# Kernel tuning notes

Measured on AMD Instinct MI355X. Metric: run time of the kernel, lower is better.

The kernel has to match this reference:

```python
import jax, jax.numpy as jnp
import numpy as np

B, H, W, K = 256, 28, 28, 5

def grid_edges_np(nb, h, w):
    # directed 8-neighbor edges on an h x w grid, replicated for nb graphs
    idx = np.arange(h * w).reshape(h, w)
    src_l, dst_l = [], []
    for dy in (-1, 0, 1):
        for dx in (-1, 0, 1):
            if dy == 0 and dx == 0:
                continue
            s = idx[max(0, -dy):h - max(0, dy), max(0, -dx):w - max(0, dx)]
            d = idx[max(0, dy):h - max(0, -dy), max(0, dx):w - max(0, -dx)]
            src_l.append(s.ravel()); dst_l.append(d.ravel())
    e = np.stack([np.concatenate(src_l), np.concatenate(dst_l)])
    off = np.arange(nb) * h * w
    return (e[:, None, :] + off[None, :, None]).reshape(2, -1).astype(np.int32)

def cart_pseudo(pos, src, dst):
    # CartesianAdj: relative offsets normalized into [0,1]^2
    cart = pos[dst] - pos[src]
    return cart / (2.0 * jnp.max(jnp.abs(cart))) + 0.5

def spline_conv(x, src, dst, pseudo, Wk, root, bias):
    # SplineConv, dim=2, kernel_size=K, degree-1 open B-splines, mean aggregation
    n = x.shape[0]
    v = jnp.clip(pseudo, 0.0, 1.0) * (K - 1)
    i0 = jnp.clip(jnp.floor(v), 0, K - 1).astype(jnp.int32)
    frac = v - i0.astype(v.dtype)
    i1 = jnp.minimum(i0 + 1, K - 1)
    Y = jnp.einsum('nf,kfg->nkg', x, Wk)  # [N, K*K, Fout]
    msg = 0.0
    for ia, ba in ((i0[:, 0], 1.0 - frac[:, 0]), (i1[:, 0], frac[:, 0])):
        for jb, bb in ((i0[:, 1], 1.0 - frac[:, 1]), (i1[:, 1], frac[:, 1])):
            msg = msg + (ba * bb)[:, None] * Y[src, ia * K + jb]
    cnt = jax.ops.segment_sum(jnp.ones((src.shape[0],), x.dtype), dst, num_segments=n)
    agg = jax.ops.segment_sum(msg, dst, num_segments=n) / jnp.maximum(cnt, 1.0)[:, None]
    return agg + x @ root + bias

def voxel_pool(x, pos, size, gy, gx, npi):
    # voxel-grid clustering: max-pool features, mean-pool positions
    batch = jnp.repeat(jnp.arange(B), npi)
    c = jnp.floor(pos / size).astype(jnp.int32)
    c = jnp.clip(c, 0, jnp.array([gx - 1, gy - 1], dtype=jnp.int32))
    cid = batch * (gy * gx) + c[:, 1] * gx + c[:, 0]
    ns = B * gy * gx
    xp = jax.ops.segment_max(x, cid, num_segments=ns)
    cnt = jax.ops.segment_sum(jnp.ones((x.shape[0],), x.dtype), cid, num_segments=ns)
    pp = jax.ops.segment_sum(pos, cid, num_segments=ns) / cnt[:, None]
    return xp, pp

def setup_inputs():
    key = jax.random.key(0)
    ks = jax.random.split(key, 10)
    ei = grid_edges_np(B, H, W)
    yy, xx = np.meshgrid(np.arange(H), np.arange(W), indexing='ij')
    p = np.stack([xx.ravel(), yy.ravel()], 1).astype(np.float32)
    pos = np.tile(p, (B, 1))
    cart = pos[ei[1]] - pos[ei[0]]
    pseudo = (cart / (2.0 * np.abs(cart).max()) + 0.5).astype(np.float32)
    r = lambda k, s, sc: jax.random.normal(k, s, dtype=jnp.float32) * sc
    return {
        'x': jax.random.normal(ks[0], (B * H * W, 1), dtype=jnp.float32),
        'pos': jnp.asarray(pos), 'pseudo': jnp.asarray(pseudo),
        'W1': r(ks[1], (K * K, 1, 32), 0.3), 'root1': r(ks[2], (1, 32), 0.3), 'b1': jnp.zeros((32,), jnp.float32),
        'W2': r(ks[3], (K * K, 32, 64), 0.08), 'root2': r(ks[4], (32, 64), 0.08), 'b2': jnp.zeros((64,), jnp.float32),
        'W3': r(ks[5], (K * K, 64, 64), 0.06), 'root3': r(ks[6], (64, 64), 0.06), 'b3': jnp.zeros((64,), jnp.float32),
        'fc1_w': r(ks[7], (256, 128), 0.06), 'fc1_b': jnp.zeros((128,), jnp.float32),
        'fc2_w': r(ks[8], (128, 10), 0.09), 'fc2_b': jnp.zeros((10,), jnp.float32),
        'edge_index': jnp.asarray(ei),
    }

def reference(x, pos, pseudo, W1, root1, b1, W2, root2, b2, W3, root3, b3, fc1_w, fc1_b, fc2_w, fc2_b, edge_index):
    src, dst = edge_index[0], edge_index[1]
    h = jax.nn.elu(spline_conv(x, src, dst, pseudo, W1, root1, b1))
    h, pos1 = voxel_pool(h, pos, 5.0, 6, 6, H * W)            # 28x28 -> 6x6
    e1 = jnp.asarray(grid_edges_np(B, 6, 6))
    h = jax.nn.elu(spline_conv(h, e1[0], e1[1], cart_pseudo(pos1, e1[0], e1[1]), W2, root2, b2))
    h, pos2 = voxel_pool(h, pos1, 7.0, 4, 4, 36)              # 6x6 -> 4x4
    e2 = jnp.asarray(grid_edges_np(B, 4, 4))
    h = jax.nn.elu(spline_conv(h, e2[0], e2[1], cart_pseudo(pos2, e2[0], e2[1]), W3, root3, b3))
    h, _ = voxel_pool(h, pos2, 14.0, 2, 2, 16)                # dense pool -> 2x2 = 4 clusters
    h = h.reshape(B, 4 * 64)
    h = jax.nn.elu(h @ fc1_w + fc1_b)
    # dropout is identity in eval mode
    h = h @ fc2_w + fc2_b
    return jax.nn.log_softmax(h, axis=1)
```

## Files before the change

kernel.cpp:

```cpp
#include <hip/hip_runtime.h>
#include <hip/hip_bf16.h>
#include <math.h>


#define DEV __device__ __forceinline__

DEV float elu_f(float v) { return v > 0.f ? v : expm1f(v); }

DEV void corners(float p0, float p1,
                 int& k00, int& k01, int& k10, int& k11,
                 float& w00, float& w01, float& w10, float& w11) {
  float v0 = fminf(fmaxf(p0, 0.f), 1.f) * 4.f;
  float v1 = fminf(fmaxf(p1, 0.f), 1.f) * 4.f;
  int i0 = (int)v0; i0 = i0 > 4 ? 4 : i0;
  int j0 = (int)v1; j0 = j0 > 4 ? 4 : j0;
  float f0 = v0 - (float)i0;
  float f1 = v1 - (float)j0;
  int i1 = i0 + 1 > 4 ? 4 : i0 + 1;
  int j1 = j0 + 1 > 4 ? 4 : j0 + 1;
  k00 = i0 * 5 + j0; k01 = i0 * 5 + j1; k10 = i1 * 5 + j0; k11 = i1 * 5 + j1;
  w00 = (1.f - f0) * (1.f - f1); w01 = (1.f - f0) * f1;
  w10 = f0 * (1.f - f1);         w11 = f0 * f1;
}

DEV float cellpos(int c, int gw) {
  return (gw == 6) ? (c < 5 ? 2.f + 5.f * (float)c : 26.f)
                   : (c < 3 ? 2.f + 7.5f * (float)c : 24.f);
}

__constant__ int c_dys[8] = {-1, -1, -1, 0, 0, 1, 1, 1};
__constant__ int c_dxs[8] = {-1, 0, 1, -1, 1, -1, 0, 1};

__global__ __launch_bounds__(256) void s1p1_kernel(
    const float* __restrict__ xin, const float* __restrict__ W1,
    const float* __restrict__ root1, const float* __restrict__ b1,
    float* __restrict__ h1p) {
  int id = blockIdx.x * 256 + threadIdx.x;
  int g = id & 31, cell = id >> 5;
  int b = cell / 36, r = cell % 36;
  int cy = r / 6, cx = r % 6;
  int y0 = cy * 5, y1 = y0 + 5 > 28 ? 28 : y0 + 5;
  int x0 = cx * 5, x1 = x0 + 5 > 28 ? 28 : x0 + 5;
  float Wreg[8];
#pragma unroll
  for (int d = 0; d < 8; d++) {
    int k = (2 * c_dxs[d] + 2) * 5 + (2 * c_dys[d] + 2);
    Wreg[d] = W1[k * 32 + g];
  }
  float rt = root1[g], bs = b1[g];
  const float* xb = xin + b * 784;
  float vmax = -3.4e38f;
  for (int y = y0; y < y1; y++) {
    for (int x = x0; x < x1; x++) {
      float acc = 0.f;
#pragma unroll
      for (int d = 0; d < 8; d++) {
        int sy = y - c_dys[d], sx = x - c_dxs[d];
        if (sy >= 0 && sy < 28 && sx >= 0 && sx < 28)
          acc += xb[sy * 28 + sx] * Wreg[d];
      }
      float cnt = (float)((1 + (y > 0) + (y < 27)) * (1 + (x > 0) + (x < 27)) - 1);
      float v = acc * (1.f / cnt) + xb[y * 28 + x] * rt + bs;
      vmax = fmaxf(vmax, elu_f(v));
    }
  }
  h1p[cell * 32 + g] = vmax;
}

__global__ __launch_bounds__(256) void prepM_kernel(
    const float* __restrict__ W2, const float* __restrict__ root2,
    const float* __restrict__ W3, const float* __restrict__ root3,
    float* __restrict__ M2, float* __restrict__ M3) {
  int idx = blockIdx.x * 256 + threadIdx.x;
  const int L2N = 36 * 9 * 32 * 64;
  int gw, F, c, d, f, g;
  const float *W, *root;
  float inv2M;
  float* Mout;
  int oidx;
  if (idx < L2N) {
    c = idx / 18432; int rem = idx % 18432;
    d = rem / 2048; f = (rem >> 6) & 31; g = rem & 63;
    gw = 6; F = 32; W = W2; root = root2; inv2M = 0.1f; Mout = M2; oidx = idx;
  } else {
    int j = idx - L2N;
    c = j / 36864; int rem = j % 36864;
    d = rem / 4096; f = (rem >> 6) & 63; g = rem & 63;
    gw = 4; F = 64; W = W3; root = root3; inv2M = 1.f / 15.f; Mout = M3; oidx = j;
  }
  float val = 0.f;
  if (d == 8) {
    val = root[f * 64 + g];
  } else {
    int cy = c / gw, cx = c % gw;
    int sy = cy - c_dys[d], sx = cx - c_dxs[d];
    if (sy >= 0 && sy < gw && sx >= 0 && sx < gw) {
      int cnt = (1 + (cy > 0) + (cy < gw - 1)) * (1 + (cx > 0) + (cx < gw - 1)) - 1;
      float invc = 1.f / (float)cnt;
      float p0 = (cellpos(cx, gw) - cellpos(sx, gw)) * inv2M + 0.5f;
      float p1 = (cellpos(cy, gw) - cellpos(sy, gw)) * inv2M + 0.5f;
      int k00, k01, k10, k11; float w00, w01, w10, w11;
      corners(p0, p1, k00, k01, k10, k11, w00, w01, w10, w11);
      val = invc * (w00 * W[(k00 * F + f) * 64 + g] + w01 * W[(k01 * F + f) * 64 + g] +
                    w10 * W[(k10 * F + f) * 64 + g] + w11 * W[(k11 * F + f) * 64 + g]);
    }
  }
  Mout[oidx] = val;
}

__global__ __launch_bounds__(256) void gemm_cls_kernel(
    const float* __restrict__ X, const float* __restrict__ M,
    float* __restrict__ P, int per, int fshift, int NC, int dps, int gw) {
  __shared__ float At[16][64];
  __shared__ float Bt[16][64];
  __shared__ int nbL[9];
  int t = threadIdx.x;
  int b0 = blockIdx.x * 64, c = blockIdx.y, s = blockIdx.z;
  int F = 1 << fshift, fmask = F - 1;
  if (t < 9) {
    int cy = c / gw, cx = c % gw;
    int nb = c;
    if (t < 8) {
      int sy = cy - c_dys[t], sx = cx - c_dxs[t];
      nb = (sy >= 0 && sy < gw && sx >= 0 && sx < gw) ? sy * gw + sx : c;
    }
    nbL[t] = nb;
  }
  __syncthreads();

  int tx = t & 15, ty = t >> 4;
  int kqA = (t & 3) * 4, rA = t >> 2;
  int bkB = t >> 4, bnB = (t & 15) * 4;
  float acc[4][4];
#pragma unroll
  for (int i = 0; i < 4; i++)
#pragma unroll
    for (int j = 0; j < 4; j++) acc[i][j] = 0.f;

  int chunkK = dps << fshift;
  for (int k0 = 0; k0 < chunkK; k0 += 16) {
    int kA = k0 + kqA;
    int dA = s * dps + (kA >> fshift);
    int fA = kA & fmask;
    float4 xv = *(const float4*)&X[(((b0 + rA) * per + nbL[dA]) << fshift) + fA];
    int kB = k0 + bkB;
    int dB = s * dps + (kB >> fshift);
    int fB = kB & fmask;
    float4 bv = *(const float4*)&M[(size_t)(((c * 9 + dB) << fshift) + fB) * 64 + bnB];
    __syncthreads();
    At[kqA + 0][rA] = xv.x; At[kqA + 1][rA] = xv.y;
    At[kqA + 2][rA] = xv.z; At[kqA + 3][rA] = xv.w;
    *(float4*)&Bt[bkB][bnB] = bv;
    __syncthreads();
#pragma unroll
    for (int kk = 0; kk < 16; kk++) {
      float4 a = *(const float4*)&At[kk][ty * 4];
      float4 bb = *(const float4*)&Bt[kk][tx * 4];
      acc[0][0] += a.x * bb.x; acc[0][1] += a.x * bb.y; acc[0][2] += a.x * bb.z; acc[0][3] += a.x * bb.w;
      acc[1][0] += a.y * bb.x; acc[1][1] += a.y * bb.y; acc[1][2] += a.y * bb.z; acc[1][3] += a.y * bb.w;
      acc[2][0] += a.z * bb.x; acc[2][1] += a.z * bb.y; acc[2][2] += a.z * bb.z; acc[2][3] += a.z * bb.w;
      acc[3][0] += a.w * bb.x; acc[3][1] += a.w * bb.y; acc[3][2] += a.w * bb.z; acc[3][3] += a.w * bb.w;
    }
  }
  float* Pq = P + ((size_t)(s * NC + c) * 256 + b0) * 64;
#pragma unroll
  for (int i = 0; i < 4; i++) {
    float4 v = {acc[i][0], acc[i][1], acc[i][2], acc[i][3]};
    *(float4*)&Pq[(size_t)(ty * 4 + i) * 64 + tx * 4] = v;
  }
}

__global__ __launch_bounds__(256) void redpool2_kernel(
    const float* __restrict__ P, const float* __restrict__ bias,
    float* __restrict__ h2p) {
  int id = blockIdx.x * 256 + threadIdx.x;
  int g = id & 63, s2 = id >> 6;
  int b = s2 >> 4, r = s2 & 15;
  int oy = r >> 2, ox = r & 3;
  int ys = oy == 0 ? 0 : (oy == 1 ? 1 : (oy == 2 ? 3 : 4));
  int yn = (oy == 1 || oy == 3) ? 2 : 1;
  int xs = ox == 0 ? 0 : (ox == 1 ? 1 : (ox == 2 ? 3 : 4));
  int xn = (ox == 1 || ox == 3) ? 2 : 1;
  float bg = bias[g];
  const size_t CS = (size_t)36 * 256 * 64;
  float vmax = -3.4e38f;
  for (int yy = ys; yy < ys + yn; yy++)
    for (int xx = xs; xx < xs + xn; xx++) {
      size_t e = (size_t)((yy * 6 + xx) * 256 + b) * 64 + g;
      float v = P[e] + P[CS + e] + P[2 * CS + e] + bg;
      vmax = fmaxf(vmax, elu_f(v));
    }
  h2p[(size_t)s2 * 64 + g] = vmax;
}

__global__ __launch_bounds__(256) void redpool3_kernel(
    const float* __restrict__ P, const float* __restrict__ bias,
    float* __restrict__ h3p) {
  int id = blockIdx.x * 256 + threadIdx.x;
  int g = id & 63, s2 = id >> 6;
  int b = s2 >> 2, r = s2 & 3;
  int oy = r >> 1, ox = r & 1;
  float bg = bias[g];
  const size_t CS = (size_t)16 * 256 * 64;
  float vmax = -3.4e38f;
#pragma unroll
  for (int i = 0; i < 2; i++)
#pragma unroll
    for (int j = 0; j < 2; j++) {
      int cy = oy * 2 + i, cx = ox * 2 + j;
      size_t e = (size_t)((cy * 4 + cx) * 256 + b) * 64 + g;
      float v = bg;
#pragma unroll
      for (int q = 0; q < 9; q++) v += P[q * CS + e];
      vmax = fmaxf(vmax, elu_f(v));
    }
  h3p[(size_t)s2 * 64 + g] = vmax;
}

__global__ __launch_bounds__(128) void fc_head_kernel(
    const float* __restrict__ h3p, const float* __restrict__ fc1w,
    const float* __restrict__ fc1b, const float* __restrict__ fc2w,
    const float* __restrict__ fc2b, float* __restrict__ out) {
  __shared__ float Al[256];
  __shared__ float h4l[128];
  __shared__ float lg[10];
  int b = blockIdx.x, t = threadIdx.x;
  Al[t] = h3p[b * 256 + t];
  Al[t + 128] = h3p[b * 256 + 128 + t];
  __syncthreads();
  float acc = fc1b[t];
  for (int k = 0; k < 256; k++) acc += Al[k] * fc1w[k * 128 + t];
  h4l[t] = elu_f(acc);
  __syncthreads();
  if (t < 10) {
    float l = fc2b[t];
    for (int k = 0; k < 128; k++) l += h4l[k] * fc2w[k * 10 + t];
    lg[t] = l;
  }
  __syncthreads();
  if (t < 10) {
    float m = lg[0];
#pragma unroll
    for (int j = 1; j < 10; j++) m = fmaxf(m, lg[j]);
    float ssum = 0.f;
#pragma unroll
    for (int j = 0; j < 10; j++) ssum += expf(lg[j] - m);
    out[b * 10 + t] = lg[t] - m - logf(ssum);
  }
}

extern "C" void kernel_launch(void* const* d_in, const int* in_sizes, int n_in,
                              void* d_out, int out_size, void* d_ws, size_t ws_size,
                              hipStream_t stream) {
  const float* x     = (const float*)d_in[0];
  const float* W1    = (const float*)d_in[3];
  const float* root1 = (const float*)d_in[4];
  const float* b1    = (const float*)d_in[5];
  const float* W2    = (const float*)d_in[6];
  const float* root2 = (const float*)d_in[7];
  const float* b2    = (const float*)d_in[8];
  const float* W3    = (const float*)d_in[9];
  const float* root3 = (const float*)d_in[10];
  const float* b3    = (const float*)d_in[11];
  const float* fc1w  = (const float*)d_in[12];
  const float* fc1b  = (const float*)d_in[13];
  const float* fc2w  = (const float*)d_in[14];
  const float* fc2b  = (const float*)d_in[15];
  float* out = (float*)d_out;

  float* ws = (float*)d_ws;
  size_t o = 0;
  float* w_h1p = ws + o; o += (size_t)9216 * 32;
  float* w_M2  = ws + o; o += (size_t)36 * 9 * 32 * 64;
  float* w_M3  = ws + o; o += (size_t)16 * 9 * 64 * 64;
  float* w_P   = ws + o; o += (size_t)9 * 16 * 256 * 64;
  float* w_h2p = ws + o; o += (size_t)4096 * 64;
  float* w_h3p = ws + o; o += (size_t)1024 * 64;

  s1p1_kernel<<<1152, 256, 0, stream>>>(x, W1, root1, b1, w_h1p);
  prepM_kernel<<<4896, 256, 0, stream>>>(W2, root2, W3, root3, w_M2, w_M3);
  gemm_cls_kernel<<<dim3(4, 36, 3), 256, 0, stream>>>(w_h1p, w_M2, w_P, 36, 5, 36, 3, 6);
  redpool2_kernel<<<1024, 256, 0, stream>>>(w_P, b2, w_h2p);
  gemm_cls_kernel<<<dim3(4, 16, 9), 256, 0, stream>>>(w_h2p, w_M3, w_P, 16, 6, 16, 1, 4);
  redpool3_kernel<<<256, 256, 0, stream>>>(w_P, b3, w_h3p);
  fc_head_kernel<<<256, 128, 0, stream>>>(w_h3p, fc1w, fc1b, fc2w, fc2b, out);
}
```

Before: 176.7 us.

## Fuse all network stages into one cooperative persistent kernel with grid barriers

Replaces the seven separate kernel launches with a single cooperatively launched persistent kernel that loops over the work of each stage and separates stages with a software grid barrier built on atomics. The redpool3 and FC head stages are merged per batch so the pooled features stay in shared memory instead of going through a global buffer. The aim is to remove per-launch overhead and inter-kernel gaps. In exchange it adds a hipMemsetAsync, an occupancy query on every call, spin-wait barriers, and lower parallelism in stages whose work exceeds the resident grid size.

```diff
diff --git a/kernel.cpp b/kernel.cpp
--- a/kernel.cpp
+++ b/kernel.cpp
@@ -1,5 +1,4 @@
 #include <hip/hip_runtime.h>
-#include <hip/hip_bf16.h>
 #include <math.h>
 
 
@@ -31,11 +30,85 @@
 __constant__ int c_dys[8] = {-1, -1, -1, 0, 0, 1, 1, 1};
 __constant__ int c_dxs[8] = {-1, 0, 1, -1, 1, -1, 0, 1};
 
-__global__ __launch_bounds__(256) void s1p1_kernel(
-    const float* __restrict__ xin, const float* __restrict__ W1,
-    const float* __restrict__ root1, const float* __restrict__ b1,
-    float* __restrict__ h1p) {
-  int id = blockIdx.x * 256 + threadIdx.x;
+DEV void gbar(unsigned* bar, int NB) {
+  __syncthreads();
+  if (threadIdx.x == 0) {
+    __threadfence();
+    unsigned g = atomicAdd(&bar[1], 0u);
+    unsigned prev = atomicAdd(&bar[0], 1u);
+    if (prev == (unsigned)(NB - 1)) {
+      atomicExch(&bar[0], 0u);
+      __threadfence();
+      atomicAdd(&bar[1], 1u);
+    } else {
+      while (atomicAdd(&bar[1], 0u) == g) { __builtin_amdgcn_s_sleep(8); }
+    }
+    __threadfence();
+  }
+  __syncthreads();
+}
+
+DEV void gemm_cls_dev(float* At, float* Bt, int* nbL,
+                      const float* __restrict__ X, const float* __restrict__ M,
+                      float* __restrict__ P,
+                      int b0, int c, int s, int per, int fshift, int NC,
+                      int dps, int gw, int t) {
+  int F = 1 << fshift, fmask = F - 1;
+  if (t < 9) {
+    int cy = c / gw, cx = c % gw;
+    int nb = c;
+    if (t < 8) {
+      int sy = cy - c_dys[t], sx = cx - c_dxs[t];
+      nb = (sy >= 0 && sy < gw && sx >= 0 && sx < gw) ? sy * gw + sx : c;
+    }
+    nbL[t] = nb;
+  }
+  __syncthreads();
+  int tx = t & 15, ty = t >> 4;
+  int kqA = (t & 3) * 4, rA = t >> 2;
+  int bkB = t >> 4, bnB = (t & 15) * 4;
+  float acc[4][4];
+#pragma unroll
+  for (int i = 0; i < 4; i++)
+#pragma unroll
+    for (int j = 0; j < 4; j++) acc[i][j] = 0.f;
+
+  int chunkK = dps << fshift;
+  for (int k0 = 0; k0 < chunkK; k0 += 16) {
+    int kA = k0 + kqA;
+    int dA = s * dps + (kA >> fshift);
+    int fA = kA & fmask;
+    float4 xv = *(const float4*)&X[(((b0 + rA) * per + nbL[dA]) << fshift) + fA];
+    int kB = k0 + bkB;
+    int dB = s * dps + (kB >> fshift);
+    int fB = kB & fmask;
+    float4 bv = *(const float4*)&M[(size_t)(((c * 9 + dB) << fshift) + fB) * 64 + bnB];
+    __syncthreads();
+    At[(kqA + 0) * 64 + rA] = xv.x; At[(kqA + 1) * 64 + rA] = xv.y;
+    At[(kqA + 2) * 64 + rA] = xv.z; At[(kqA + 3) * 64 + rA] = xv.w;
+    *(float4*)&Bt[bkB * 64 + bnB] = bv;
+    __syncthreads();
+#pragma unroll
+    for (int kk = 0; kk < 16; kk++) {
+      float4 a = *(const float4*)&At[kk * 64 + ty * 4];
+      float4 bb = *(const float4*)&Bt[kk * 64 + tx * 4];
+      acc[0][0] += a.x * bb.x; acc[0][1] += a.x * bb.y; acc[0][2] += a.x * bb.z; acc[0][3] += a.x * bb.w;
+      acc[1][0] += a.y * bb.x; acc[1][1] += a.y * bb.y; acc[1][2] += a.y * bb.z; acc[1][3] += a.y * bb.w;
+      acc[2][0] += a.z * bb.x; acc[2][1] += a.z * bb.y; acc[2][2] += a.z * bb.z; acc[2][3] += a.z * bb.w;
+      acc[3][0] += a.w * bb.x; acc[3][1] += a.w * bb.y; acc[3][2] += a.w * bb.z; acc[3][3] += a.w * bb.w;
+    }
+  }
+  float* Pq = P + ((size_t)(s * NC + c) * 256 + b0) * 64;
+#pragma unroll
+  for (int i = 0; i < 4; i++) {
+    float4 v = {acc[i][0], acc[i][1], acc[i][2], acc[i][3]};
+    *(float4*)&Pq[(size_t)(ty * 4 + i) * 64 + tx * 4] = v;
+  }
+}
+
+DEV void s1p1_body(int id, const float* __restrict__ xin,
+                   const float* __restrict__ W1, const float* __restrict__ root1,
+                   const float* __restrict__ b1, float* __restrict__ h1p) {
   int g = id & 31, cell = id >> 5;
   int b = cell / 36, r = cell % 36;
   int cy = r / 6, cx = r % 6;
@@ -67,25 +140,22 @@
   h1p[cell * 32 + g] = vmax;
 }
 
-__global__ __launch_bounds__(256) void prepM_kernel(
-    const float* __restrict__ W2, const float* __restrict__ root2,
-    const float* __restrict__ W3, const float* __restrict__ root3,
-    float* __restrict__ M2, float* __restrict__ M3) {
-  int idx = blockIdx.x * 256 + threadIdx.x;
+DEV void prepM_body(int idx, const float* __restrict__ W2, const float* __restrict__ root2,
+                    const float* __restrict__ W3, const float* __restrict__ root3,
+                    float* __restrict__ M2, float* __restrict__ M3) {
   const int L2N = 36 * 9 * 32 * 64;
-  int gw, F, c, d, f, g;
+  int gw, F, c, d, f, g, oidx;
   const float *W, *root;
   float inv2M;
   float* Mout;
-  int oidx;
   if (idx < L2N) {
     c = idx / 18432; int rem = idx % 18432;
-    d = rem / 2048; f = (rem >> 6) & 31; g = rem & 63;
+    d = rem / 2048; f = (rem >> 6) & 31; g = idx & 63;
     gw = 6; F = 32; W = W2; root = root2; inv2M = 0.1f; Mout = M2; oidx = idx;
   } else {
     int j = idx - L2N;
     c = j / 36864; int rem = j % 36864;
-    d = rem / 4096; f = (rem >> 6) & 63; g = rem & 63;
+    d = rem / 4096; f = (rem >> 6) & 63; g = j & 63;
     gw = 4; F = 64; W = W3; root = root3; inv2M = 1.f / 15.f; Mout = M3; oidx = j;
   }
   float val = 0.f;
@@ -108,72 +178,8 @@
   Mout[oidx] = val;
 }
 
-__global__ __launch_bounds__(256) void gemm_cls_kernel(
-    const float* __restrict__ X, const float* __restrict__ M,
-    float* __restrict__ P, int per, int fshift, int NC, int dps, int gw) {
-  __shared__ float At[16][64];
-  __shared__ float Bt[16][64];
-  __shared__ int nbL[9];
-  int t = threadIdx.x;
-  int b0 = blockIdx.x * 64, c = blockIdx.y, s = blockIdx.z;
-  int F = 1 << fshift, fmask = F - 1;
-  if (t < 9) {
-    int cy = c / gw, cx = c % gw;
-    int nb = c;
-    if (t < 8) {
-      int sy = cy - c_dys[t], sx = cx - c_dxs[t];
-      nb = (sy >= 0 && sy < gw && sx >= 0 && sx < gw) ? sy * gw + sx : c;
-    }
-    nbL[t] = nb;
-  }
-  __syncthreads();
-
-  int tx = t & 15, ty = t >> 4;
-  int kqA = (t & 3) * 4, rA = t >> 2;
-  int bkB = t >> 4, bnB = (t & 15) * 4;
-  float acc[4][4];
-#pragma unroll
-  for (int i = 0; i < 4; i++)
-#pragma unroll
-    for (int j = 0; j < 4; j++) acc[i][j] = 0.f;
-
-  int chunkK = dps << fshift;
-  for (int k0 = 0; k0 < chunkK; k0 += 16) {
-    int kA = k0 + kqA;
-    int dA = s * dps + (kA >> fshift);
-    int fA = kA & fmask;
-    float4 xv = *(const float4*)&X[(((b0 + rA) * per + nbL[dA]) << fshift) + fA];
-    int kB = k0 + bkB;
-    int dB = s * dps + (kB >> fshift);
-    int fB = kB & fmask;
-    float4 bv = *(const float4*)&M[(size_t)(((c * 9 + dB) << fshift) + fB) * 64 + bnB];
-    __syncthreads();
-    At[kqA + 0][rA] = xv.x; At[kqA + 1][rA] = xv.y;
-    At[kqA + 2][rA] = xv.z; At[kqA + 3][rA] = xv.w;
-    *(float4*)&Bt[bkB][bnB] = bv;
-    __syncthreads();
-#pragma unroll
-    for (int kk = 0; kk < 16; kk++) {
-      float4 a = *(const float4*)&At[kk][ty * 4];
-      float4 bb = *(const float4*)&Bt[kk][tx * 4];
-      acc[0][0] += a.x * bb.x; acc[0][1] += a.x * bb.y; acc[0][2] += a.x * bb.z; acc[0][3] += a.x * bb.w;
-      acc[1][0] += a.y * bb.x; acc[1][1] += a.y * bb.y; acc[1][2] += a.y * bb.z; acc[1][3] += a.y * bb.w;
-      acc[2][0] += a.z * bb.x; acc[2][1] += a.z * bb.y; acc[2][2] += a.z * bb.z; acc[2][3] += a.z * bb.w;
-      acc[3][0] += a.w * bb.x; acc[3][1] += a.w * bb.y; acc[3][2] += a.w * bb.z; acc[3][3] += a.w * bb.w;
-    }
-  }
-  float* Pq = P + ((size_t)(s * NC + c) * 256 + b0) * 64;
-#pragma unroll
-  for (int i = 0; i < 4; i++) {
-    float4 v = {acc[i][0], acc[i][1], acc[i][2], acc[i][3]};
-    *(float4*)&Pq[(size_t)(ty * 4 + i) * 64 + tx * 4] = v;
-  }
-}
-
-__global__ __launch_bounds__(256) void redpool2_kernel(
-    const float* __restrict__ P, const float* __restrict__ bias,
-    float* __restrict__ h2p) {
-  int id = blockIdx.x * 256 + threadIdx.x;
+DEV void redpool2_body(int id, const float* __restrict__ P,
+                       const float* __restrict__ bias, float* __restrict__ h2p) {
   int g = id & 63, s2 = id >> 6;
   int b = s2 >> 4, r = s2 & 15;
   int oy = r >> 2, ox = r & 3;
@@ -191,6 +197,121 @@
       vmax = fmaxf(vmax, elu_f(v));
     }
   h2p[(size_t)s2 * 64 + g] = vmax;
+}
+
+__global__ __launch_bounds__(256) void fused_net_kernel(
+    const float* __restrict__ xin,
+    const float* __restrict__ W1, const float* __restrict__ root1, const float* __restrict__ b1,
+    const float* __restrict__ W2, const float* __restrict__ root2, const float* __restrict__ b2,
+    const float* __restrict__ W3, const float* __restrict__ root3, const float* __restrict__ b3,
+    const float* __restrict__ fc1w, const float* __restrict__ fc1b,
+    const float* __restrict__ fc2w, const float* __restrict__ fc2b,
+    float* __restrict__ out,
+    float* __restrict__ h1p, float* __restrict__ M2, float* __restrict__ M3,
+    float* __restrict__ P, float* __restrict__ h2p,
+    unsigned* bar, int NB) {
+  __shared__ __align__(16) float smem[2048];
+  __shared__ int nbL[9];
+  int t = threadIdx.x, bid = blockIdx.x;
+  int TOT = NB * 256;
+
+  for (int vb = bid; vb < 1152; vb += NB)
+    s1p1_body(vb * 256 + t, xin, W1, root1, b1, h1p);
+  for (int idx = bid * 256 + t; idx < 1253376; idx += TOT)
+    prepM_body(idx, W2, root2, W3, root3, M2, M3);
+  gbar(bar, NB);
+
+  for (int tile = bid; tile < 432; tile += NB)
+    gemm_cls_dev(smem, smem + 1024, nbL, h1p, M2, P,
+                 (tile & 3) * 64, (tile >> 2) % 36, tile / 144, 36, 5, 36, 3, 6, t);
+  gbar(bar, NB);
+
+  for (int id = bid * 256 + t; id < 262144; id += TOT)
+    redpool2_body(id, P, b2, h2p);
+  gbar(bar, NB);
+
+  for (int tile = bid; tile < 576; tile += NB)
+    gemm_cls_dev(smem, smem + 1024, nbL, h2p, M3, P,
+                 (tile & 3) * 64, (tile >> 2) & 15, tile >> 6, 16, 6, 16, 1, 4, t);
+  gbar(bar, NB);
+
+  for (int bb = bid; bb < 256; bb += NB) {
+    float* Al = smem;
+    float* h4l = smem + 256;
+    float* lg = smem + 384;
+    {
+      int r = t >> 6, g = t & 63;
+      int oy = r >> 1, ox = r & 1;
+      float bg = b3[g];
+      const size_t CS = (size_t)16 * 256 * 64;
+      float vmax = -3.4e38f;
+#pragma unroll
+      for (int i = 0; i < 2; i++)
+#pragma unroll
+        for (int j = 0; j < 2; j++) {
+          int cy = oy * 2 + i, cx = ox * 2 + j;
+          size_t e = (size_t)((cy * 4 + cx) * 256 + bb) * 64 + g;
+          float v = bg;
+#pragma unroll
+          for (int q = 0; q < 9; q++) v += P[q * CS + e];
+          vmax = fmaxf(vmax, elu_f(v));
+        }
+      __syncthreads();
+      Al[t] = vmax;
+    }
+    __syncthreads();
+    if (t < 128) {
+      float acc = fc1b[t];
+      for (int k = 0; k < 256; k++) acc += Al[k] * fc1w[k * 128 + t];
+      h4l[t] = elu_f(acc);
+    }
+    __syncthreads();
+    if (t < 10) {
+      float l = fc2b[t];
+      for (int k = 0; k < 128; k++) l += h4l[k] * fc2w[k * 10 + t];
+      lg[t] = l;
+    }
+    __syncthreads();
+    if (t < 10) {
+      float m = lg[0];
+#pragma unroll
+      for (int j = 1; j < 10; j++) m = fmaxf(m, lg[j]);
+      float ssum = 0.f;
+#pragma unroll
+      for (int j = 0; j < 10; j++) ssum += expf(lg[j] - m);
+      out[bb * 10 + t] = lg[t] - m - logf(ssum);
+    }
+  }
+}
+
+__global__ __launch_bounds__(256) void s1p1_kernel(
+    const float* __restrict__ xin, const float* __restrict__ W1,
+    const float* __restrict__ root1, const float* __restrict__ b1,
+    float* __restrict__ h1p) {
+  s1p1_body(blockIdx.x * 256 + threadIdx.x, xin, W1, root1, b1, h1p);
+}
+
+__global__ __launch_bounds__(256) void prepM_kernel(
+    const float* __restrict__ W2, const float* __restrict__ root2,
+    const float* __restrict__ W3, const float* __restrict__ root3,
+    float* __restrict__ M2, float* __restrict__ M3) {
+  prepM_body(blockIdx.x * 256 + threadIdx.x, W2, root2, W3, root3, M2, M3);
+}
+
+__global__ __launch_bounds__(256) void gemm_cls_kernel(
+    const float* __restrict__ X, const float* __restrict__ M,
+    float* __restrict__ P, int per, int fshift, int NC, int dps, int gw) {
+  __shared__ __align__(16) float smem[2048];
+  __shared__ int nbL[9];
+  gemm_cls_dev(smem, smem + 1024, nbL, X, M, P,
+               blockIdx.x * 64, blockIdx.y, blockIdx.z, per, fshift, NC, dps, gw,
+               threadIdx.x);
+}
+
+__global__ __launch_bounds__(256) void redpool2_kernel(
+    const float* __restrict__ P, const float* __restrict__ bias,
+    float* __restrict__ h2p) {
+  redpool2_body(blockIdx.x * 256 + threadIdx.x, P, bias, h2p);
 }
 
 __global__ __launch_bounds__(256) void redpool3_kernel(
@@ -276,12 +397,40 @@
   float* w_P   = ws + o; o += (size_t)9 * 16 * 256 * 64;
   float* w_h2p = ws + o; o += (size_t)4096 * 64;
   float* w_h3p = ws + o; o += (size_t)1024 * 64;
-
-  s1p1_kernel<<<1152, 256, 0, stream>>>(x, W1, root1, b1, w_h1p);
-  prepM_kernel<<<4896, 256, 0, stream>>>(W2, root2, W3, root3, w_M2, w_M3);
-  gemm_cls_kernel<<<dim3(4, 36, 3), 256, 0, stream>>>(w_h1p, w_M2, w_P, 36, 5, 36, 3, 6);
-  redpool2_kernel<<<1024, 256, 0, stream>>>(w_P, b2, w_h2p);
-  gemm_cls_kernel<<<dim3(4, 16, 9), 256, 0, stream>>>(w_h2p, w_M3, w_P, 16, 6, 16, 1, 4);
-  redpool3_kernel<<<256, 256, 0, stream>>>(w_P, b3, w_h3p);
-  fc_head_kernel<<<256, 128, 0, stream>>>(w_h3p, fc1w, fc1b, fc2w, fc2b, out);
-}
+  unsigned* w_bar = (unsigned*)(ws + o); o += 16;
+
+  hipMemsetAsync(w_bar, 0, 2 * sizeof(unsigned), stream);
+
+  int maxB = 0;
+  hipError_t qe = hipOccupancyMaxActiveBlocksPerMultiprocessor(
+      &maxB, (const void*)fused_net_kernel, 256, 0);
+  int NB = 576;
+  if (qe == hipSuccess && maxB > 0) {
+    int tot = maxB * 256;
+    if (tot < NB) NB = tot;
+  } else {
+    NB = 256;
+  }
+
+  void* args[] = {
+    (void*)&x,
+    (void*)&W1, (void*)&root1, (void*)&b1,
+    (void*)&W2, (void*)&root2, (void*)&b2,
+    (void*)&W3, (void*)&root3, (void*)&b3,
+    (void*)&fc1w, (void*)&fc1b, (void*)&fc2w, (void*)&fc2b,
+    (void*)&out,
+    (void*)&w_h1p, (void*)&w_M2, (void*)&w_M3, (void*)&w_P, (void*)&w_h2p,
+    (void*)&w_bar, (void*)&NB,
+  };
+  hipError_t e = hipLaunchCooperativeKernel((const void*)fused_net_kernel,
+                                            dim3(NB), dim3(256), args, 0, stream);
+  if (e != hipSuccess) {
+    s1p1_kernel<<<1152, 256, 0, stream>>>(x, W1, root1, b1, w_h1p);
+    prepM_kernel<<<4896, 256, 0, stream>>>(W2, root2, W3, root3, w_M2, w_M3);
+    gemm_cls_kernel<<<dim3(4, 36, 3), 256, 0, stream>>>(w_h1p, w_M2, w_P, 36, 5, 36, 3, 6);
+    redpool2_kernel<<<1024, 256, 0, stream>>>(w_P, b2, w_h2p);
+    gemm_cls_kernel<<<dim3(4, 16, 9), 256, 0, stream>>>(w_h2p, w_M3, w_P, 16, 6, 16, 1, 4);
+    redpool3_kernel<<<256, 256, 0, stream>>>(w_P, b3, w_h3p);
+    fc_head_kernel<<<256, 128, 0, stream>>>(w_h3p, fc1w, fc1b, fc2w, fc2b, out);
+  }
+}
```

Measured after the change: 446.5 us. +152.7%, slower.

## Fuse conv stages with pooling and drop split-K partial buffers

Applied to the files above, without the earlier changes.

Merges the stage-1 conv and weight-precompute kernels into one launch, and replaces the split-K GEMMs plus separate reduce/pool kernels with per-cell GEMMs that accumulate the full K. The conv3 kernel applies the layer-2 max-pool, bias and ELU while loading its A tile, and the head kernel does the final pool before the FC layers. This cuts launches from seven to four and removes the large partial-sum buffer round trips. In exchange the new GEMM tiles are smaller (16 rows, only 64 threads loading A, one row per thread), so arithmetic intensity and latency hiding drop, and pooled values are recomputed for every neighbour read.

```diff
diff --git a/kernel.cpp b/kernel.cpp
--- a/kernel.cpp
+++ b/kernel.cpp
@@ -1,5 +1,4 @@
 #include <hip/hip_runtime.h>
-#include <hip/hip_bf16.h>
 #include <math.h>
 
 
@@ -31,11 +30,9 @@
 __constant__ int c_dys[8] = {-1, -1, -1, 0, 0, 1, 1, 1};
 __constant__ int c_dxs[8] = {-1, 0, 1, -1, 1, -1, 0, 1};
 
-__global__ __launch_bounds__(256) void s1p1_kernel(
-    const float* __restrict__ xin, const float* __restrict__ W1,
-    const float* __restrict__ root1, const float* __restrict__ b1,
-    float* __restrict__ h1p) {
-  int id = blockIdx.x * 256 + threadIdx.x;
+DEV void s1p1_body(int id, const float* __restrict__ xin,
+                   const float* __restrict__ W1, const float* __restrict__ root1,
+                   const float* __restrict__ b1, float* __restrict__ h1p) {
   int g = id & 31, cell = id >> 5;
   int b = cell / 36, r = cell % 36;
   int cy = r / 6, cx = r % 6;
@@ -67,25 +64,22 @@
   h1p[cell * 32 + g] = vmax;
 }
 
-__global__ __launch_bounds__(256) void prepM_kernel(
-    const float* __restrict__ W2, const float* __restrict__ root2,
-    const float* __restrict__ W3, const float* __restrict__ root3,
-    float* __restrict__ M2, float* __restrict__ M3) {
-  int idx = blockIdx.x * 256 + threadIdx.x;
+DEV void prepM_body(int idx, const float* __restrict__ W2, const float* __restrict__ root2,
+                    const float* __restrict__ W3, const float* __restrict__ root3,
+                    float* __restrict__ M2, float* __restrict__ M3) {
   const int L2N = 36 * 9 * 32 * 64;
-  int gw, F, c, d, f, g;
+  int gw, F, c, d, f, g, oidx;
   const float *W, *root;
   float inv2M;
   float* Mout;
-  int oidx;
   if (idx < L2N) {
     c = idx / 18432; int rem = idx % 18432;
-    d = rem / 2048; f = (rem >> 6) & 31; g = rem & 63;
+    d = rem / 2048; f = (rem >> 6) & 31; g = idx & 63;
     gw = 6; F = 32; W = W2; root = root2; inv2M = 0.1f; Mout = M2; oidx = idx;
   } else {
     int j = idx - L2N;
     c = j / 36864; int rem = j % 36864;
-    d = rem / 4096; f = (rem >> 6) & 63; g = rem & 63;
+    d = rem / 4096; f = (rem >> 6) & 63; g = j & 63;
     gw = 4; F = 64; W = W3; root = root3; inv2M = 1.f / 15.f; Mout = M3; oidx = j;
   }
   float val = 0.f;
@@ -108,125 +102,155 @@
   Mout[oidx] = val;
 }
 
-__global__ __launch_bounds__(256) void gemm_cls_kernel(
-    const float* __restrict__ X, const float* __restrict__ M,
-    float* __restrict__ P, int per, int fshift, int NC, int dps, int gw) {
-  __shared__ float At[16][64];
+__global__ __launch_bounds__(256) void stageA_kernel(
+    const float* __restrict__ xin, const float* __restrict__ W1,
+    const float* __restrict__ root1, const float* __restrict__ b1,
+    const float* __restrict__ W2, const float* __restrict__ root2,
+    const float* __restrict__ W3, const float* __restrict__ root3,
+    float* __restrict__ h1p, float* __restrict__ M2, float* __restrict__ M3) {
+  int bid = blockIdx.x, t = threadIdx.x;
+  if (bid < 1152) {
+    s1p1_body(bid * 256 + t, xin, W1, root1, b1, h1p);
+  } else {
+    prepM_body((bid - 1152) * 256 + t, W2, root2, W3, root3, M2, M3);
+  }
+}
+
+__global__ __launch_bounds__(256) void conv2_kernel(
+    const float* __restrict__ h1p, const float* __restrict__ M2,
+    float* __restrict__ h2raw) {
+  __shared__ float At[16][17];
   __shared__ float Bt[16][64];
   __shared__ int nbL[9];
   int t = threadIdx.x;
-  int b0 = blockIdx.x * 64, c = blockIdx.y, s = blockIdx.z;
-  int F = 1 << fshift, fmask = F - 1;
+  int b0 = blockIdx.x * 16, c = blockIdx.y;
   if (t < 9) {
-    int cy = c / gw, cx = c % gw;
+    int cy = c / 6, cx = c % 6;
     int nb = c;
     if (t < 8) {
       int sy = cy - c_dys[t], sx = cx - c_dxs[t];
-      nb = (sy >= 0 && sy < gw && sx >= 0 && sx < gw) ? sy * gw + sx : c;
+      nb = (sy >= 0 && sy < 6 && sx >= 0 && sx < 6) ? sy * 6 + sx : c;
     }
     nbL[t] = nb;
   }
   __syncthreads();
-
   int tx = t & 15, ty = t >> 4;
-  int kqA = (t & 3) * 4, rA = t >> 2;
-  int bkB = t >> 4, bnB = (t & 15) * 4;
-  float acc[4][4];
-#pragma unroll
-  for (int i = 0; i < 4; i++)
-#pragma unroll
-    for (int j = 0; j < 4; j++) acc[i][j] = 0.f;
-
-  int chunkK = dps << fshift;
-  for (int k0 = 0; k0 < chunkK; k0 += 16) {
-    int kA = k0 + kqA;
-    int dA = s * dps + (kA >> fshift);
-    int fA = kA & fmask;
-    float4 xv = *(const float4*)&X[(((b0 + rA) * per + nbL[dA]) << fshift) + fA];
-    int kB = k0 + bkB;
-    int dB = s * dps + (kB >> fshift);
-    int fB = kB & fmask;
-    float4 bv = *(const float4*)&M[(size_t)(((c * 9 + dB) << fshift) + fB) * 64 + bnB];
+  int mA = t >> 2, fqA = (t & 3) * 4;
+  float acc[4] = {0.f, 0.f, 0.f, 0.f};
+  for (int k0 = 0; k0 < 288; k0 += 16) {
+    int dA = k0 >> 5, fb = k0 & 31;
+    float4 xv = {0.f, 0.f, 0.f, 0.f};
+    if (t < 64)
+      xv = *(const float4*)&h1p[((b0 + mA) * 36 + nbL[dA]) * 32 + fb + fqA];
+    float4 bv = *(const float4*)&M2[(size_t)((c * 9 + dA) * 32 + fb + ty) * 64 + tx * 4];
     __syncthreads();
-    At[kqA + 0][rA] = xv.x; At[kqA + 1][rA] = xv.y;
-    At[kqA + 2][rA] = xv.z; At[kqA + 3][rA] = xv.w;
-    *(float4*)&Bt[bkB][bnB] = bv;
+    if (t < 64) {
+      At[fqA + 0][mA] = xv.x; At[fqA + 1][mA] = xv.y;
+      At[fqA + 2][mA] = xv.z; At[fqA + 3][mA] = xv.w;
+    }
+    *(float4*)&Bt[ty][tx * 4] = bv;
     __syncthreads();
 #pragma unroll
     for (int kk = 0; kk < 16; kk++) {
-      float4 a = *(const float4*)&At[kk][ty * 4];
+      float a = At[kk][ty];
       float4 bb = *(const float4*)&Bt[kk][tx * 4];
-      acc[0][0] += a.x * bb.x; acc[0][1] += a.x * bb.y; acc[0][2] += a.x * bb.z; acc[0][3] += a.x * bb.w;
-      acc[1][0] += a.y * bb.x; acc[1][1] += a.y * bb.y; acc[1][2] += a.y * bb.z; acc[1][3] += a.y * bb.w;
-      acc[2][0] += a.z * bb.x; acc[2][1] += a.z * bb.y; acc[2][2] += a.z * bb.z; acc[2][3] += a.z * bb.w;
-      acc[3][0] += a.w * bb.x; acc[3][1] += a.w * bb.y; acc[3][2] += a.w * bb.z; acc[3][3] += a.w * bb.w;
-    }
-  }
-  float* Pq = P + ((size_t)(s * NC + c) * 256 + b0) * 64;
-#pragma unroll
-  for (int i = 0; i < 4; i++) {
-    float4 v = {acc[i][0], acc[i][1], acc[i][2], acc[i][3]};
-    *(float4*)&Pq[(size_t)(ty * 4 + i) * 64 + tx * 4] = v;
-  }
-}
-
-__global__ __launch_bounds__(256) void redpool2_kernel(
-    const float* __restrict__ P, const float* __restrict__ bias,
-    float* __restrict__ h2p) {
-  int id = blockIdx.x * 256 + threadIdx.x;
-  int g = id & 63, s2 = id >> 6;
-  int b = s2 >> 4, r = s2 & 15;
-  int oy = r >> 2, ox = r & 3;
-  int ys = oy == 0 ? 0 : (oy == 1 ? 1 : (oy == 2 ? 3 : 4));
-  int yn = (oy == 1 || oy == 3) ? 2 : 1;
-  int xs = ox == 0 ? 0 : (ox == 1 ? 1 : (ox == 2 ? 3 : 4));
-  int xn = (ox == 1 || ox == 3) ? 2 : 1;
-  float bg = bias[g];
-  const size_t CS = (size_t)36 * 256 * 64;
-  float vmax = -3.4e38f;
-  for (int yy = ys; yy < ys + yn; yy++)
-    for (int xx = xs; xx < xs + xn; xx++) {
-      size_t e = (size_t)((yy * 6 + xx) * 256 + b) * 64 + g;
-      float v = P[e] + P[CS + e] + P[2 * CS + e] + bg;
-      vmax = fmaxf(vmax, elu_f(v));
-    }
-  h2p[(size_t)s2 * 64 + g] = vmax;
-}
-
-__global__ __launch_bounds__(256) void redpool3_kernel(
-    const float* __restrict__ P, const float* __restrict__ bias,
-    float* __restrict__ h3p) {
-  int id = blockIdx.x * 256 + threadIdx.x;
-  int g = id & 63, s2 = id >> 6;
-  int b = s2 >> 2, r = s2 & 3;
-  int oy = r >> 1, ox = r & 1;
-  float bg = bias[g];
-  const size_t CS = (size_t)16 * 256 * 64;
-  float vmax = -3.4e38f;
-#pragma unroll
-  for (int i = 0; i < 2; i++)
-#pragma unroll
-    for (int j = 0; j < 2; j++) {
-      int cy = oy * 2 + i, cx = ox * 2 + j;
-      size_t e = (size_t)((cy * 4 + cx) * 256 + b) * 64 + g;
-      float v = bg;
-#pragma unroll
-      for (int q = 0; q < 9; q++) v += P[q * CS + e];
-      vmax = fmaxf(vmax, elu_f(v));
-    }
-  h3p[(size_t)s2 * 64 + g] = vmax;
-}
-
-__global__ __launch_bounds__(128) void fc_head_kernel(
-    const float* __restrict__ h3p, const float* __restrict__ fc1w,
-    const float* __restrict__ fc1b, const float* __restrict__ fc2w,
-    const float* __restrict__ fc2b, float* __restrict__ out) {
+      acc[0] += a * bb.x; acc[1] += a * bb.y;
+      acc[2] += a * bb.z; acc[3] += a * bb.w;
+    }
+  }
+  float4 v = {acc[0], acc[1], acc[2], acc[3]};
+  *(float4*)&h2raw[((size_t)(b0 + ty) * 36 + c) * 64 + tx * 4] = v;
+}
+
+__global__ __launch_bounds__(256) void conv3_kernel(
+    const float* __restrict__ h2raw, const float* __restrict__ M3,
+    const float* __restrict__ b2, float* __restrict__ h3raw) {
+  __shared__ float At[16][17];
+  __shared__ float Bt[16][64];
+  __shared__ int nbC[9][4];
+  __shared__ float b2l[64];
+  int t = threadIdx.x;
+  int b0 = blockIdx.x * 16, c = blockIdx.y;
+  if (t < 64) b2l[t] = b2[t];
+  if (t < 9) {
+    int cy = c >> 2, cx = c & 3;
+    int cc = c;
+    if (t < 8) {
+      int sy = cy - c_dys[t], sx = cx - c_dxs[t];
+      cc = (sy >= 0 && sy < 4 && sx >= 0 && sx < 4) ? sy * 4 + sx : c;
+    }
+    int oy = cc >> 2, ox = cc & 3;
+    int ys = oy == 0 ? 0 : (oy == 1 ? 1 : (oy == 2 ? 3 : 4));
+    int yn = (oy == 1 || oy == 3) ? 2 : 1;
+    int xs = ox == 0 ? 0 : (ox == 1 ? 1 : (ox == 2 ? 3 : 4));
+    int xn = (ox == 1 || ox == 3) ? 2 : 1;
+    int cl[4]; int idx = 0;
+    for (int yy = ys; yy < ys + yn; yy++)
+      for (int xx = xs; xx < xs + xn; xx++) cl[idx++] = yy * 6 + xx;
+    for (int i = idx; i < 4; i++) cl[i] = cl[0];
+    nbC[t][0] = cl[0]; nbC[t][1] = cl[1]; nbC[t][2] = cl[2]; nbC[t][3] = cl[3];
+  }
+  __syncthreads();
+  int tx = t & 15, ty = t >> 4;
+  int mA = t >> 2, fqA = (t & 3) * 4;
+  float acc[4] = {0.f, 0.f, 0.f, 0.f};
+  for (int k0 = 0; k0 < 576; k0 += 16) {
+    int dA = k0 >> 6, fb = k0 & 63;
+    float4 av = {0.f, 0.f, 0.f, 0.f};
+    if (t < 64) {
+      const float* base = &h2raw[(size_t)(b0 + mA) * 36 * 64 + fb + fqA];
+      float4 v0 = *(const float4*)&base[nbC[dA][0] * 64];
+      float4 v1 = *(const float4*)&base[nbC[dA][1] * 64];
+      float4 v2 = *(const float4*)&base[nbC[dA][2] * 64];
+      float4 v3 = *(const float4*)&base[nbC[dA][3] * 64];
+      int f = fb + fqA;
+      av.x = elu_f(fmaxf(fmaxf(v0.x, v1.x), fmaxf(v2.x, v3.x)) + b2l[f + 0]);
+      av.y = elu_f(fmaxf(fmaxf(v0.y, v1.y), fmaxf(v2.y, v3.y)) + b2l[f + 1]);
+      av.z = elu_f(fmaxf(fmaxf(v0.z, v1.z), fmaxf(v2.z, v3.z)) + b2l[f + 2]);
+      av.w = elu_f(fmaxf(fmaxf(v0.w, v1.w), fmaxf(v2.w, v3.w)) + b2l[f + 3]);
+    }
+    float4 bv = *(const float4*)&M3[(size_t)((c * 9 + dA) * 64 + fb + ty) * 64 + tx * 4];
+    __syncthreads();
+    if (t < 64) {
+      At[fqA + 0][mA] = av.x; At[fqA + 1][mA] = av.y;
+      At[fqA + 2][mA] = av.z; At[fqA + 3][mA] = av.w;
+    }
+    *(float4*)&Bt[ty][tx * 4] = bv;
+    __syncthreads();
+#pragma unroll
+    for (int kk = 0; kk < 16; kk++) {
+      float a = At[kk][ty];
+      float4 bb = *(const float4*)&Bt[kk][tx * 4];
+      acc[0] += a * bb.x; acc[1] += a * bb.y;
+      acc[2] += a * bb.z; acc[3] += a * bb.w;
+    }
+  }
+  float4 v = {acc[0], acc[1], acc[2], acc[3]};
+  *(float4*)&h3raw[((size_t)(b0 + ty) * 16 + c) * 64 + tx * 4] = v;
+}
+
+__global__ __launch_bounds__(128) void head_kernel(
+    const float* __restrict__ h3raw, const float* __restrict__ b3,
+    const float* __restrict__ fc1w, const float* __restrict__ fc1b,
+    const float* __restrict__ fc2w, const float* __restrict__ fc2b,
+    float* __restrict__ out) {
   __shared__ float Al[256];
   __shared__ float h4l[128];
   __shared__ float lg[10];
   int b = blockIdx.x, t = threadIdx.x;
-  Al[t] = h3p[b * 256 + t];
-  Al[t + 128] = h3p[b * 256 + 128 + t];
+  for (int e = t; e < 256; e += 128) {
+    int r = e >> 6, g = e & 63;
+    int oy = r >> 1, ox = r & 1;
+    float vmax = -3.4e38f;
+#pragma unroll
+    for (int i = 0; i < 2; i++)
+#pragma unroll
+      for (int j = 0; j < 2; j++) {
+        int cell = (oy * 2 + i) * 4 + (ox * 2 + j);
+        vmax = fmaxf(vmax, h3raw[((size_t)b * 16 + cell) * 64 + g]);
+      }
+    Al[e] = elu_f(vmax + b3[g]);
+  }
   __syncthreads();
   float acc = fc1b[t];
   for (int k = 0; k < 256; k++) acc += Al[k] * fc1w[k * 128 + t];
@@ -270,18 +294,15 @@
 
   float* ws = (float*)d_ws;
   size_t o = 0;
-  float* w_h1p = ws + o; o += (size_t)9216 * 32;
-  float* w_M2  = ws + o; o += (size_t)36 * 9 * 32 * 64;
-  float* w_M3  = ws + o; o += (size_t)16 * 9 * 64 * 64;
-  float* w_P   = ws + o; o += (size_t)9 * 16 * 256 * 64;
-  float* w_h2p = ws + o; o += (size_t)4096 * 64;
-  float* w_h3p = ws + o; o += (size_t)1024 * 64;
-
-  s1p1_kernel<<<1152, 256, 0, stream>>>(x, W1, root1, b1, w_h1p);
-  prepM_kernel<<<4896, 256, 0, stream>>>(W2, root2, W3, root3, w_M2, w_M3);
-  gemm_cls_kernel<<<dim3(4, 36, 3), 256, 0, stream>>>(w_h1p, w_M2, w_P, 36, 5, 36, 3, 6);
-  redpool2_kernel<<<1024, 256, 0, stream>>>(w_P, b2, w_h2p);
-  gemm_cls_kernel<<<dim3(4, 16, 9), 256, 0, stream>>>(w_h2p, w_M3, w_P, 16, 6, 16, 1, 4);
-  redpool3_kernel<<<256, 256, 0, stream>>>(w_P, b3, w_h3p);
-  fc_head_kernel<<<256, 128, 0, stream>>>(w_h3p, fc1w, fc1b, fc2w, fc2b, out);
-}
+  float* w_h1p   = ws + o; o += (size_t)9216 * 32;
+  float* w_M2    = ws + o; o += (size_t)36 * 9 * 32 * 64;
+  float* w_M3    = ws + o; o += (size_t)16 * 9 * 64 * 64;
+  float* w_h2raw = ws + o; o += (size_t)256 * 36 * 64;
+  float* w_h3raw = ws + o; o += (size_t)256 * 16 * 64;
+
+  stageA_kernel<<<6048, 256, 0, stream>>>(x, W1, root1, b1, W2, root2, W3, root3,
+                                          w_h1p, w_M2, w_M3);
+  conv2_kernel<<<dim3(16, 36), 256, 0, stream>>>(w_h1p, w_M2, w_h2raw);
+  conv3_kernel<<<dim3(16, 16), 256, 0, stream>>>(w_h2raw, w_M3, b2, w_h3raw);
+  head_kernel<<<256, 128, 0, stream>>>(w_h3raw, b3, fc1w, fc1b, fc2w, fc2b, out);
+}
```

Result: slower. 204.2 us (+15.6%).
